# Optimization experiments

Measured on AMD Instinct MI355X. Metric: run time of the kernel, lower is better.

## Reference

```python
import jax, jax.numpy as jnp
import numpy as np

N_SAMPLES = 4194304
N_RAYS = 65536


def setup_inputs() -> dict:
    key = jax.random.key(0)
    k1, k2, k3 = jax.random.split(key, 3)
    rgb_samples = jax.random.uniform(k1, (N_SAMPLES, 3), dtype=jnp.float32)
    weights_samples = jax.random.uniform(k2, (N_SAMPLES, 1), dtype=jnp.float32)
    ray_indices = jnp.sort(jax.random.randint(k3, (N_SAMPLES,), 0, N_RAYS, dtype=jnp.int32))
    return {
        "rgb_samples": rgb_samples,
        "weights_samples": weights_samples,
        "ray_indices": ray_indices,
        "n_rays": N_RAYS,
    }


def reference(rgb_samples, weights_samples, ray_indices, n_rays):
    # Packed/ragged per-ray weighted color integration:
    # pred_rgb[r] = sum_{i in ray r} weights[i] * rgb[i]
    weighted = rgb_samples * weights_samples  # [N_samples, 3]
    pred_rgb = jax.ops.segment_sum(weighted, ray_indices, num_segments=n_rays)  # [N_rays, 3]
    return pred_rgb
```

## Files before the change

kernel.cpp:

```cpp
#include <hip/hip_runtime.h>


#define SPL 4
#define TILE_SAMPLES (64 * SPL)
#define TPW 8

struct Tile {
    int   ids[SPL];
    float ws[SPL], sx[SPL], sy[SPL], sz[SPL];
};

__device__ __forceinline__ void load_tile(const float* __restrict__ rgb,
                                          const float* __restrict__ w,
                                          const int*   __restrict__ idx,
                                          int tbase, int lane, int n,
                                          Tile& T)
{
    const int base = tbase + lane * SPL;
    if (base + SPL <= n) {
        int4   i0 = *(const int4*)(idx + base);
        float4 w0 = *(const float4*)(w + base);
        const float4* r4 = (const float4*)(rgb + 3 * base);
        float4 r0 = r4[0], r1 = r4[1], r2 = r4[2];

        T.ids[0]=i0.x; T.ids[1]=i0.y; T.ids[2]=i0.z; T.ids[3]=i0.w;
        T.ws[0]=w0.x; T.ws[1]=w0.y; T.ws[2]=w0.z; T.ws[3]=w0.w;
        T.sx[0]=r0.x; T.sy[0]=r0.y; T.sz[0]=r0.z;
        T.sx[1]=r0.w; T.sy[1]=r1.x; T.sz[1]=r1.y;
        T.sx[2]=r1.z; T.sy[2]=r1.w; T.sz[2]=r2.x;
        T.sx[3]=r2.y; T.sy[3]=r2.z; T.sz[3]=r2.w;
    } else {
        #pragma unroll
        for (int k = 0; k < SPL; ++k) {
            int  s  = base + k;
            bool ok = (s < n);
            int  sc = ok ? s : (n - 1);
            T.ids[k] = idx[sc];
            T.ws[k]  = ok ? w[sc] : 0.0f;
            T.sx[k] = rgb[3*sc+0]; T.sy[k] = rgb[3*sc+1]; T.sz[k] = rgb[3*sc+2];
        }
    }
}

__device__ __forceinline__ void process_tile(const Tile& T, int lane,
                                             float* __restrict__ out)
{
    const int first = T.ids[0];
    int   cur = first;
    float ax = T.ws[0]*T.sx[0], ay = T.ws[0]*T.sy[0], az = T.ws[0]*T.sz[0];
    float hx = 0.f, hy = 0.f, hz = 0.f;
    bool  f = false;
    #pragma unroll
    for (int k = 1; k < SPL; ++k) {
        if (T.ids[k] != cur) {
            if (!f) { hx = ax; hy = ay; hz = az; f = true; }
            else {
                atomicAdd(&out[cur*3+0], ax);
                atomicAdd(&out[cur*3+1], ay);
                atomicAdd(&out[cur*3+2], az);
            }
            ax = ay = az = 0.f;
            cur = T.ids[k];
        }
        ax = fmaf(T.ws[k], T.sx[k], ax);
        ay = fmaf(T.ws[k], T.sy[k], ay);
        az = fmaf(T.ws[k], T.sz[k], az);
    }
    const int t_id = cur;

    int  t_prev = __shfl_up(t_id, 1);
    bool edge   = (lane > 0) && (t_prev != first);
    bool brk    = f || edge;
    unsigned long long bm = __ballot(brk);

    bool term  = f && !edge;
    int   nt   = __shfl_down((int)term, 1);
    float nhx  = __shfl_down(hx, 1);
    float nhy  = __shfl_down(hy, 1);
    float nhz  = __shfl_down(hz, 1);
    bool  absb = (lane < 63) && nt;
    float Sx = ax + (absb ? nhx : 0.f);
    float Sy = ay + (absb ? nhy : 0.f);
    float Sz = az + (absb ? nhz : 0.f);

    #pragma unroll
    for (int d = 1; d < 64; d <<= 1) {
        float ox = __shfl_down(Sx, d);
        float oy = __shfl_down(Sy, d);
        float oz = __shfl_down(Sz, d);
        unsigned long long between = ((bm >> 1) >> lane) & ((1ull << d) - 1ull);
        bool cont = (lane + d < 64) && (between == 0);
        if (cont) { Sx += ox; Sy += oy; Sz += oz; }
    }

    if (lane == 0 || brk) {
        atomicAdd(&out[t_id*3+0], Sx);
        atomicAdd(&out[t_id*3+1], Sy);
        atomicAdd(&out[t_id*3+2], Sz);
    }
    if (f && (edge || lane == 0)) {
        atomicAdd(&out[first*3+0], hx);
        atomicAdd(&out[first*3+1], hy);
        atomicAdd(&out[first*3+2], hz);
    }
}

__global__ __launch_bounds__(256, 2) void integrate_kernel(
    const float* __restrict__ rgb,
    const float* __restrict__ w,
    const int*   __restrict__ idx,
    float*       __restrict__ out,
    int n)
{
    const int lane = threadIdx.x & 63;
    const int wave = (int)(((unsigned)blockIdx.x * blockDim.x + threadIdx.x) >> 6);
    const int b0 = wave * (TPW * TILE_SAMPLES);
    if (b0 >= n) return;

    Tile T[TPW];
    bool h[TPW];
    #pragma unroll
    for (int t = 0; t < TPW; ++t) {
        int bt = b0 + t * TILE_SAMPLES;
        h[t] = (bt < n);
        if (h[t]) load_tile(rgb, w, idx, bt, lane, n, T[t]);
    }
    #pragma unroll
    for (int t = 0; t < TPW; ++t) {
        if (h[t]) process_tile(T[t], lane, out);
    }
}

extern "C" void kernel_launch(void* const* d_in, const int* in_sizes, int n_in,
                              void* d_out, int out_size, void* d_ws, size_t ws_size,
                              hipStream_t stream) {
    const float* rgb = (const float*)d_in[0];
    const float* w   = (const float*)d_in[1];
    const int*   idx = (const int*)  d_in[2];
    float*       out = (float*)d_out;

    int n = in_sizes[2];


    long long spw    = (long long)TPW * TILE_SAMPLES;
    long long waves  = ((long long)n + spw - 1) / spw;
    long long blocks = (waves + 3) / 4;
    integrate_kernel<<<(int)blocks, 256, 0, stream>>>(rgb, w, idx, out, n);
}
```

Before: 114.3 us.

## Replace wave segmented scan with block-level LDS accumulator and ray-offset slots

Drops the per-wave segmented shuffle scan. Each thread flushes its per-ray partial sums into a shared-memory accumulator indexed by ray minus the block's first ray, falling back to global atomics when a ray lands outside the slot window. After a barrier, the block writes non-zero slots to global memory with one atomic per slot. Tiles per wave are halved and the occupancy hint is raised. This cuts global atomic traffic but adds contended LDS atomics and two block barriers.

```diff
diff --git a/kernel.cpp b/kernel.cpp
--- a/kernel.cpp
+++ b/kernel.cpp
@@ -3,7 +3,10 @@
 
 #define SPL 4
 #define TILE_SAMPLES (64 * SPL)
-#define TPW 8
+#define TPW 4
+#define WAVES_PER_BLOCK 4
+#define BLOCK_SAMPLES (WAVES_PER_BLOCK * TPW * TILE_SAMPLES)
+#define SLOTS 512
 
 struct Tile {
     int   ids[SPL];
@@ -42,23 +45,33 @@
     }
 }
 
-__device__ __forceinline__ void process_tile(const Tile& T, int lane,
+__device__ __forceinline__ void flush_piece(int ray, int rmin,
+                                            float ax, float ay, float az,
+                                            float* acc,
+                                            float* __restrict__ out)
+{
+    const int slot = ray - rmin;
+    if (slot < SLOTS) {
+        atomicAdd(&acc[slot*3+0], ax);
+        atomicAdd(&acc[slot*3+1], ay);
+        atomicAdd(&acc[slot*3+2], az);
+    } else {
+        atomicAdd(&out[ray*3+0], ax);
+        atomicAdd(&out[ray*3+1], ay);
+        atomicAdd(&out[ray*3+2], az);
+    }
+}
+
+__device__ __forceinline__ void process_tile(const Tile& T, int rmin,
+                                             float* acc,
                                              float* __restrict__ out)
 {
-    const int first = T.ids[0];
-    int   cur = first;
+    int   cur = T.ids[0];
     float ax = T.ws[0]*T.sx[0], ay = T.ws[0]*T.sy[0], az = T.ws[0]*T.sz[0];
-    float hx = 0.f, hy = 0.f, hz = 0.f;
-    bool  f = false;
     #pragma unroll
     for (int k = 1; k < SPL; ++k) {
         if (T.ids[k] != cur) {
-            if (!f) { hx = ax; hy = ay; hz = az; f = true; }
-            else {
-                atomicAdd(&out[cur*3+0], ax);
-                atomicAdd(&out[cur*3+1], ay);
-                atomicAdd(&out[cur*3+2], az);
-            }
+            flush_piece(cur, rmin, ax, ay, az, acc, out);
             ax = ay = az = 0.f;
             cur = T.ids[k];
         }
@@ -66,57 +79,27 @@
         ay = fmaf(T.ws[k], T.sy[k], ay);
         az = fmaf(T.ws[k], T.sz[k], az);
     }
-    const int t_id = cur;
-
-    int  t_prev = __shfl_up(t_id, 1);
-    bool edge   = (lane > 0) && (t_prev != first);
-    bool brk    = f || edge;
-    unsigned long long bm = __ballot(brk);
-
-    bool term  = f && !edge;
-    int   nt   = __shfl_down((int)term, 1);
-    float nhx  = __shfl_down(hx, 1);
-    float nhy  = __shfl_down(hy, 1);
-    float nhz  = __shfl_down(hz, 1);
-    bool  absb = (lane < 63) && nt;
-    float Sx = ax + (absb ? nhx : 0.f);
-    float Sy = ay + (absb ? nhy : 0.f);
-    float Sz = az + (absb ? nhz : 0.f);
-
-    #pragma unroll
-    for (int d = 1; d < 64; d <<= 1) {
-        float ox = __shfl_down(Sx, d);
-        float oy = __shfl_down(Sy, d);
-        float oz = __shfl_down(Sz, d);
-        unsigned long long between = ((bm >> 1) >> lane) & ((1ull << d) - 1ull);
-        bool cont = (lane + d < 64) && (between == 0);
-        if (cont) { Sx += ox; Sy += oy; Sz += oz; }
-    }
-
-    if (lane == 0 || brk) {
-        atomicAdd(&out[t_id*3+0], Sx);
-        atomicAdd(&out[t_id*3+1], Sy);
-        atomicAdd(&out[t_id*3+2], Sz);
-    }
-    if (f && (edge || lane == 0)) {
-        atomicAdd(&out[first*3+0], hx);
-        atomicAdd(&out[first*3+1], hy);
-        atomicAdd(&out[first*3+2], hz);
-    }
+    flush_piece(cur, rmin, ax, ay, az, acc, out);
 }
 
-__global__ __launch_bounds__(256, 2) void integrate_kernel(
+__global__ __launch_bounds__(256, 4) void integrate_kernel(
     const float* __restrict__ rgb,
     const float* __restrict__ w,
     const int*   __restrict__ idx,
     float*       __restrict__ out,
     int n)
 {
-    const int lane = threadIdx.x & 63;
-    const int wave = (int)(((unsigned)blockIdx.x * blockDim.x + threadIdx.x) >> 6);
-    const int b0 = wave * (TPW * TILE_SAMPLES);
-    if (b0 >= n) return;
+    __shared__ float acc[SLOTS * 3];
 
+    const int tid  = threadIdx.x;
+    const int lane = tid & 63;
+    const int wid  = tid >> 6;
+    const int blk0 = blockIdx.x * BLOCK_SAMPLES;
+    const bool blk_live = (blk0 < n);
+
+    const int rmin = blk_live ? idx[blk0] : 0;
+
+    const int b0 = blk0 + wid * (TPW * TILE_SAMPLES);
     Tile T[TPW];
     bool h[TPW];
     #pragma unroll
@@ -125,9 +108,22 @@
         h[t] = (bt < n);
         if (h[t]) load_tile(rgb, w, idx, bt, lane, n, T[t]);
     }
+
+    for (int i = tid; i < SLOTS * 3; i += 256) acc[i] = 0.f;
+
+    __syncthreads();
+
     #pragma unroll
-    for (int t = 0; t < TPW; ++t) {
-        if (h[t]) process_tile(T[t], lane, out);
+    for (int t = 0; t < TPW; ++t)
+        if (h[t]) process_tile(T[t], rmin, acc, out);
+
+    __syncthreads();
+
+    if (blk_live) {
+        for (int i = tid; i < SLOTS * 3; i += 256) {
+            float v = acc[i];
+            if (v != 0.f) atomicAdd(&out[rmin * 3 + i], v);
+        }
     }
 }
 
@@ -142,8 +138,6 @@
     int n = in_sizes[2];
 
 
-    long long spw    = (long long)TPW * TILE_SAMPLES;
-    long long waves  = ((long long)n + spw - 1) / spw;
-    long long blocks = (waves + 3) / 4;
+    long long blocks = ((long long)n + BLOCK_SAMPLES - 1) / BLOCK_SAMPLES;
     integrate_kernel<<<(int)blocks, 256, 0, stream>>>(rgb, w, idx, out, n);
 }
```

Measured after the change: 121.1 us. 5.9% more time.

## Stage RGB tile loads directly into LDS and shrink per-wave tiles

Applied to the files above, without the earlier changes.

Moves the per-lane RGB loads into LDS with direct global-to-LDS loads, then reads them back as float4 after waiting on outstanding loads. Tiles per wave drop from 8 to 2 and the occupancy hint rises from 2 to 4 blocks per CU. The aim is to cut vector register pressure and raise the number of waves keeping loads in flight. The cost is LDS traffic and LDS allocation, plus a hard wait on all outstanding loads before processing.

```diff
diff --git a/kernel.cpp b/kernel.cpp
--- a/kernel.cpp
+++ b/kernel.cpp
@@ -3,42 +3,63 @@
 
 #define SPL 4
 #define TILE_SAMPLES (64 * SPL)
-#define TPW 8
+#define TPW 2
+#define WAVES_PER_BLOCK 4
+#define BLOCK_SAMPLES (WAVES_PER_BLOCK * TPW * TILE_SAMPLES)
+#define RGB_TILE_FLOATS (64 * 12)
+
+#define AS1 __attribute__((address_space(1)))
+#define AS3 __attribute__((address_space(3)))
 
 struct Tile {
     int   ids[SPL];
     float ws[SPL], sx[SPL], sy[SPL], sz[SPL];
 };
 
-__device__ __forceinline__ void load_tile(const float* __restrict__ rgb,
+__device__ __forceinline__ void post_tile(const float* __restrict__ rgb,
                                           const float* __restrict__ w,
                                           const int*   __restrict__ idx,
-                                          int tbase, int lane, int n,
-                                          Tile& T)
+                                          float* lds_rgb,
+                                          int tbase, int lane, Tile& T)
 {
     const int base = tbase + lane * SPL;
-    if (base + SPL <= n) {
-        int4   i0 = *(const int4*)(idx + base);
-        float4 w0 = *(const float4*)(w + base);
-        const float4* r4 = (const float4*)(rgb + 3 * base);
-        float4 r0 = r4[0], r1 = r4[1], r2 = r4[2];
+    int4   i0 = *(const int4*)(idx + base);
+    float4 w0 = *(const float4*)(w + base);
+    T.ids[0]=i0.x; T.ids[1]=i0.y; T.ids[2]=i0.z; T.ids[3]=i0.w;
+    T.ws[0]=w0.x;  T.ws[1]=w0.y;  T.ws[2]=w0.z;  T.ws[3]=w0.w;
 
-        T.ids[0]=i0.x; T.ids[1]=i0.y; T.ids[2]=i0.z; T.ids[3]=i0.w;
-        T.ws[0]=w0.x; T.ws[1]=w0.y; T.ws[2]=w0.z; T.ws[3]=w0.w;
-        T.sx[0]=r0.x; T.sy[0]=r0.y; T.sz[0]=r0.z;
-        T.sx[1]=r0.w; T.sy[1]=r1.x; T.sz[1]=r1.y;
-        T.sx[2]=r1.z; T.sy[2]=r1.w; T.sz[2]=r2.x;
-        T.sx[3]=r2.y; T.sy[3]=r2.z; T.sz[3]=r2.w;
-    } else {
-        #pragma unroll
-        for (int k = 0; k < SPL; ++k) {
-            int  s  = base + k;
-            bool ok = (s < n);
-            int  sc = ok ? s : (n - 1);
-            T.ids[k] = idx[sc];
-            T.ws[k]  = ok ? w[sc] : 0.0f;
-            T.sx[k] = rgb[3*sc+0]; T.sy[k] = rgb[3*sc+1]; T.sz[k] = rgb[3*sc+2];
-        }
+    const float* gsrc = rgb + 3 * tbase + lane * 12;
+    __builtin_amdgcn_global_load_lds((AS1 const void*)(gsrc + 0), (AS3 void*)(lds_rgb +   0), 16, 0, 0);
+    __builtin_amdgcn_global_load_lds((AS1 const void*)(gsrc + 4), (AS3 void*)(lds_rgb + 256), 16, 0, 0);
+    __builtin_amdgcn_global_load_lds((AS1 const void*)(gsrc + 8), (AS3 void*)(lds_rgb + 512), 16, 0, 0);
+}
+
+__device__ __forceinline__ void finish_tile(const float* lds_rgb, int lane, Tile& T)
+{
+    float4 r0 = *(const float4*)(lds_rgb +   0 + lane * 4);
+    float4 r1 = *(const float4*)(lds_rgb + 256 + lane * 4);
+    float4 r2 = *(const float4*)(lds_rgb + 512 + lane * 4);
+    T.sx[0]=r0.x; T.sy[0]=r0.y; T.sz[0]=r0.z;
+    T.sx[1]=r0.w; T.sy[1]=r1.x; T.sz[1]=r1.y;
+    T.sx[2]=r1.z; T.sy[2]=r1.w; T.sz[2]=r2.x;
+    T.sx[3]=r2.y; T.sy[3]=r2.z; T.sz[3]=r2.w;
+}
+
+__device__ __forceinline__ void load_tile_slow(const float* __restrict__ rgb,
+                                               const float* __restrict__ w,
+                                               const int*   __restrict__ idx,
+                                               int tbase, int lane, int n,
+                                               Tile& T)
+{
+    const int base = tbase + lane * SPL;
+    #pragma unroll
+    for (int k = 0; k < SPL; ++k) {
+        int  s  = base + k;
+        bool ok = (s < n);
+        int  sc = ok ? s : (n - 1);
+        T.ids[k] = idx[sc];
+        T.ws[k]  = ok ? w[sc] : 0.0f;
+        T.sx[k] = rgb[3*sc+0]; T.sy[k] = rgb[3*sc+1]; T.sz[k] = rgb[3*sc+2];
     }
 }
 
@@ -105,29 +126,42 @@
     }
 }
 
-__global__ __launch_bounds__(256, 2) void integrate_kernel(
+__global__ __launch_bounds__(256, 4) void integrate_kernel(
     const float* __restrict__ rgb,
     const float* __restrict__ w,
     const int*   __restrict__ idx,
     float*       __restrict__ out,
     int n)
 {
-    const int lane = threadIdx.x & 63;
-    const int wave = (int)(((unsigned)blockIdx.x * blockDim.x + threadIdx.x) >> 6);
-    const int b0 = wave * (TPW * TILE_SAMPLES);
+    __shared__ float rgbbuf[WAVES_PER_BLOCK * TPW * RGB_TILE_FLOATS];
+
+    const int tid  = threadIdx.x;
+    const int lane = tid & 63;
+    const int wid  = tid >> 6;
+    const int b0   = blockIdx.x * BLOCK_SAMPLES + wid * (TPW * TILE_SAMPLES);
     if (b0 >= n) return;
 
     Tile T[TPW];
-    bool h[TPW];
+    bool h[TPW], fast[TPW];
     #pragma unroll
     for (int t = 0; t < TPW; ++t) {
-        int bt = b0 + t * TILE_SAMPLES;
-        h[t] = (bt < n);
-        if (h[t]) load_tile(rgb, w, idx, bt, lane, n, T[t]);
+        const int tb = b0 + t * TILE_SAMPLES;
+        h[t]    = (tb < n);
+        fast[t] = (tb + TILE_SAMPLES <= n);
+        if (!h[t]) continue;
+        float* lr = &rgbbuf[(wid * TPW + t) * RGB_TILE_FLOATS];
+        if (fast[t]) post_tile(rgb, w, idx, lr, tb, lane, T[t]);
+        else         load_tile_slow(rgb, w, idx, tb, lane, n, T[t]);
     }
+
+    asm volatile("s_waitcnt vmcnt(0)" ::: "memory");
+
     #pragma unroll
     for (int t = 0; t < TPW; ++t) {
-        if (h[t]) process_tile(T[t], lane, out);
+        if (!h[t]) continue;
+        if (fast[t])
+            finish_tile(&rgbbuf[(wid * TPW + t) * RGB_TILE_FLOATS], lane, T[t]);
+        process_tile(T[t], lane, out);
     }
 }
 
@@ -142,8 +176,6 @@
     int n = in_sizes[2];
 
 
-    long long spw    = (long long)TPW * TILE_SAMPLES;
-    long long waves  = ((long long)n + spw - 1) / spw;
-    long long blocks = (waves + 3) / 4;
+    long long blocks = ((long long)n + BLOCK_SAMPLES - 1) / BLOCK_SAMPLES;
     integrate_kernel<<<(int)blocks, 256, 0, stream>>>(rgb, w, idx, out, n);
 }
```

New measurement: 106.8 us. -6.6%, faster.
